# Performance work log

Measured on AMD Instinct MI355X. Metric: run time of the kernel, lower is better.

## Reference

```python
import math
import jax, jax.numpy as jnp
import numpy as np


def setup_inputs() -> dict:
    key = jax.random.key(0)
    T, C = 8192, 2048
    layer_depth, num_layers = 5, 10
    ks = jax.random.split(key, 8)

    x = jax.random.normal(ks[0], (T, C), jnp.float32)
    sx = jax.random.normal(ks[1], (C,), jnp.float32)
    aa = jnp.zeros((C,), jnp.float32)
    bb = jnp.zeros((C,), jnp.float32)
    pp = jnp.zeros((C,), jnp.float32)

    # parameter initial values per TimeMix.setup
    r01 = layer_depth / (num_layers - 1)
    r10 = 1.0 - layer_depth / num_layers
    zigzag = 0.5 * (jnp.arange(1, C + 1) % 3 - 1).astype(jnp.float32)
    time_first = jnp.full((C,), math.log(0.3), jnp.float32) + zigzag
    h = jnp.arange(C, dtype=jnp.float32)
    time_decay = (-5.0 + 8.0 * (h / (C - 1)) ** (0.7 + 1.3 * r01)).astype(jnp.float32)
    xr = jnp.arange(C, dtype=jnp.float32) / C
    time_mix_k = xr ** r10
    time_mix_v = time_mix_k + 0.3 * r01
    time_mix_r = xr ** (0.5 * r10)

    ln_scale = jnp.ones((C,), jnp.float32)
    ln_bias = jnp.zeros((C,), jnp.float32)

    s = 1.0 / np.sqrt(C)  # lecun-normal-ish scale for Dense kernels
    Wk = jax.random.normal(ks[2], (C, C), jnp.float32) * s
    Wv = jax.random.normal(ks[3], (C, C), jnp.float32) * s
    Wr = jax.random.normal(ks[4], (C, C), jnp.float32) * s
    Wo = jax.random.normal(ks[5], (C, C), jnp.float32) * s

    return dict(x=x, sx=sx, aa=aa, bb=bb, pp=pp,
                time_first=time_first, time_decay=time_decay,
                time_mix_k=time_mix_k, time_mix_v=time_mix_v, time_mix_r=time_mix_r,
                ln_scale=ln_scale, ln_bias=ln_bias,
                Wk=Wk, Wv=Wv, Wr=Wr, Wo=Wo)


def reference(x, sx, aa, bb, pp, time_first, time_decay,
              time_mix_k, time_mix_v, time_mix_r,
              ln_scale, ln_bias, Wk, Wv, Wr, Wo):
    # LayerNorm(eps=1e-5)
    mu = jnp.mean(x, axis=-1, keepdims=True)
    var = jnp.var(x, axis=-1, keepdims=True)
    xx = (x - mu) * jax.lax.rsqrt(var + 1e-5) * ln_scale + ln_bias  # [T, C]

    # token shift: previous timestep (sx state for t=0)
    sxs = jnp.concatenate((sx[None, :], xx[:-1, :]), axis=0)  # [T, C]
    kx = xx * time_mix_k + sxs * (1.0 - time_mix_k)
    vx = xx * time_mix_v + sxs * (1.0 - time_mix_v)
    rx = xx * time_mix_r + sxs * (1.0 - time_mix_r)

    r = jax.nn.sigmoid(rx @ Wr)  # [T, C]
    k = kx @ Wk                  # [T, C]
    v = vx @ Wv                  # [T, C]

    w = -jnp.exp(time_decay)     # [C]

    def step(state, kv):
        aa, bb, pp = state
        kk, vv = kv
        # output with numerically-stable log-sum-exp style bookkeeping
        ww = time_first + kk
        p = jnp.maximum(pp, ww)
        e1 = jnp.exp(pp - p)
        e2 = jnp.exp(ww - p)
        out = ((e1 * aa + e2 * vv) / (e1 * bb + e2)).astype(r.dtype)
        # state update
        ww2 = w + pp
        p2 = jnp.maximum(ww2, kk)
        e1b = jnp.exp(ww2 - p2)
        e2b = jnp.exp(kk - p2)
        aa = e1b * aa + e2b * vv
        bb = e1b * bb + e2b
        return (aa, bb, p2), out

    (aa, bb, pp), wkv = jax.lax.scan(step, (aa, bb, pp), (k, v))  # wkv: [T, C]

    out = x + (r * wkv) @ Wo
    return (out, xx[-1, :], aa, bb, pp)
```

## Files before the change

kernel.cpp:

```cpp
#include <hip/hip_runtime.h>
#include <stdint.h>

#define T_DIM 8192
#define C_DIM 2048
#define LCHUNK 128
#define NCHUNK (T_DIM / LCHUNK)

typedef unsigned short u16;
typedef __bf16 bf16x8_t __attribute__((ext_vector_type(8)));
typedef float f32x4_t __attribute__((ext_vector_type(4)));

__device__ __forceinline__ u16 f2bf(float f) {
    union { float f; uint32_t u; } x; x.f = f;
    uint32_t r = x.u + 0x7fffu + ((x.u >> 16) & 1u);
    return (u16)(r >> 16);
}
__device__ __forceinline__ float bf2f(u16 u) {
    union { uint32_t u; float f; } x; x.u = ((uint32_t)u) << 16;
    return x.f;
}
__device__ __forceinline__ void gload16(const void* g, void* l) {
    __builtin_amdgcn_global_load_lds((const __attribute__((address_space(1))) uint32_t*)g,
                                     (__attribute__((address_space(3))) uint32_t*)l, 16, 0, 0);
}
__device__ __forceinline__ f32x4_t mfma16(bf16x8_t a, bf16x8_t b, f32x4_t c) {
    return __builtin_amdgcn_mfma_f32_16x16x32_bf16(a, b, c, 0, 0, 0);
}

__device__ __forceinline__ void transpose_tile(const float* __restrict__ W, u16* __restrict__ Tm,
                                               int bn, int bk, float* shf)
{
    const int tid = threadIdx.x;
    const int tx = tid & 31, ty = tid >> 5;
#pragma unroll
    for (int i = 0; i < 4; ++i)
        shf[(ty + 8 * i) * 33 + tx] = W[(size_t)(bk + ty + 8 * i) * C_DIM + bn + tx];
    __syncthreads();
#pragma unroll
    for (int i = 0; i < 4; ++i)
        Tm[(size_t)(bn + ty + 8 * i) * C_DIM + bk + tx] = f2bf(shf[tx * 33 + ty + 8 * i]);
}

union F8 { float4 v[2]; float f[8]; };

__global__ __launch_bounds__(256)
void prep_kernel(const float* __restrict__ W0, const float* __restrict__ W1,
                 const float* __restrict__ W2, u16* __restrict__ Wt,
                 const float* __restrict__ x, const float* __restrict__ sx,
                 const float* __restrict__ lns, const float* __restrict__ lnb,
                 const float* __restrict__ tmk, const float* __restrict__ tmv,
                 const float* __restrict__ tmr,
                 u16* __restrict__ kx, u16* __restrict__ vx, u16* __restrict__ rx,
                 float* __restrict__ xx_last)
{
    __shared__ float shf[32 * 33];
    const int bid = blockIdx.x;
    const int tid = threadIdx.x;

    if (bid >= 8192) {
        const int z = (bid - 8192) >> 12;
        const int rem = (bid - 8192) & 4095;
        const float* W = (z == 0) ? W0 : (z == 1) ? W1 : W2;
        transpose_tile(W, Wt + (size_t)z * C_DIM * C_DIM, (rem & 63) * 32, (rem >> 6) * 32, shf);
        return;
    }

    const int t = bid;
    const size_t rowoff = (size_t)t * C_DIM;

    F8 a, p;
    const float4* xt = (const float4*)(x + rowoff);
    a.v[0] = xt[2 * tid]; a.v[1] = xt[2 * tid + 1];
    const float4* xp = (t == 0) ? (const float4*)sx : (const float4*)(x + rowoff - C_DIM);
    p.v[0] = xp[2 * tid]; p.v[1] = xp[2 * tid + 1];

    float s1 = 0.f, s2 = 0.f, s3 = 0.f, s4 = 0.f;
#pragma unroll
    for (int i = 0; i < 8; ++i) {
        s1 += a.f[i]; s2 += a.f[i] * a.f[i];
        s3 += p.f[i]; s4 += p.f[i] * p.f[i];
    }
#pragma unroll
    for (int off = 32; off; off >>= 1) {
        s1 += __shfl_down(s1, off);
        s2 += __shfl_down(s2, off);
        s3 += __shfl_down(s3, off);
        s4 += __shfl_down(s4, off);
    }
    float* red = shf;
    if ((tid & 63) == 0) {
        red[0 * 4 + (tid >> 6)] = s1; red[1 * 4 + (tid >> 6)] = s2;
        red[2 * 4 + (tid >> 6)] = s3; red[3 * 4 + (tid >> 6)] = s4;
    }
    __syncthreads();
    s1 = red[0] + red[1] + red[2] + red[3];
    s2 = red[4] + red[5] + red[6] + red[7];
    s3 = red[8] + red[9] + red[10] + red[11];
    s4 = red[12] + red[13] + red[14] + red[15];
    const float inv = 1.0f / (float)C_DIM;
    const float mu = s1 * inv;
    const float rstd = rsqrtf(s2 * inv - mu * mu + 1e-5f);
    const float mup = s3 * inv;
    const float rstdp = rsqrtf(s4 * inv - mup * mup + 1e-5f);

    F8 ls, lb, mk, mv, mr;
    { const float4* q = (const float4*)lns; ls.v[0] = q[2*tid]; ls.v[1] = q[2*tid+1]; }
    { const float4* q = (const float4*)lnb; lb.v[0] = q[2*tid]; lb.v[1] = q[2*tid+1]; }
    { const float4* q = (const float4*)tmk; mk.v[0] = q[2*tid]; mk.v[1] = q[2*tid+1]; }
    { const float4* q = (const float4*)tmv; mv.v[0] = q[2*tid]; mv.v[1] = q[2*tid+1]; }
    { const float4* q = (const float4*)tmr; mr.v[0] = q[2*tid]; mr.v[1] = q[2*tid+1]; }

    union { u16 u[8]; uint4 q; } ok, ov, orr;
#pragma unroll
    for (int i = 0; i < 8; ++i) {
        const float xxv  = (a.f[i] - mu) * rstd * ls.f[i] + lb.f[i];
        const float prev = (t == 0) ? p.f[i] : (p.f[i] - mup) * rstdp * ls.f[i] + lb.f[i];
        ok.u[i]  = f2bf(xxv * mk.f[i] + prev * (1.f - mk.f[i]));
        ov.u[i]  = f2bf(xxv * mv.f[i] + prev * (1.f - mv.f[i]));
        orr.u[i] = f2bf(xxv * mr.f[i] + prev * (1.f - mr.f[i]));
        if (t == T_DIM - 1) xx_last[tid * 8 + i] = xxv;
    }
    ((uint4*)(kx + rowoff))[tid] = ok.q;
    ((uint4*)(vx + rowoff))[tid] = ov.q;
    ((uint4*)(rx + rowoff))[tid] = orr.q;
}

__device__ __forceinline__ void gemm_core_sb(
    const u16* __restrict__ A, const u16* __restrict__ Bt,
    void* __restrict__ Cout, const int mode, const int N, const int K,
    const int m0, const int n0, u16* lds)
{
    const int tid = threadIdx.x;
    const int wave = tid >> 6, lane = tid & 63;
    const int wm = wave >> 1, wn = wave & 1;
    const int fr = lane & 15, fo = lane >> 4;
    const int sw = (fo ^ ((fr >> 1) & 3)) * 8;

    f32x4_t acc[4][4] = {};

    const int lrow = lane >> 2;
    const int scol = ((lane & 3) ^ ((lane >> 3) & 3)) * 8;
    const u16* gA = A  + (size_t)(m0 + wave * 16 + lrow) * K + scol;
    const u16* gB = Bt + (size_t)(n0 + wave * 16 + lrow) * K + scol;
    const size_t rk64 = (size_t)64 * K;
    const int dA = wave * 512;
    const int dB = 4096 + wave * 512;

    const int NT = K >> 5;
    for (int t = 0; t < NT; ++t) {
        const u16* ga = gA + (size_t)t * 32;
        const u16* gb = gB + (size_t)t * 32;
        gload16(ga,        lds + dA);
        gload16(ga + rk64, lds + dA + 2048);
        gload16(gb,        lds + dB);
        gload16(gb + rk64, lds + dB + 2048);
        __syncthreads();
        const u16* lA = lds + (wm * 64 + fr) * 32;
        const u16* lB = lds + 4096 + (wn * 64 + fr) * 32;
        bf16x8_t a[4], b[4];
#pragma unroll
        for (int i = 0; i < 4; ++i) {
            a[i] = *(const bf16x8_t*)(lA + i * 512 + sw);
            b[i] = *(const bf16x8_t*)(lB + i * 512 + sw);
        }
        __builtin_amdgcn_s_setprio(1);
#pragma unroll
        for (int mi = 0; mi < 4; ++mi)
#pragma unroll
            for (int ni = 0; ni < 4; ++ni)
                acc[mi][ni] = mfma16(a[mi], b[ni], acc[mi][ni]);
        __builtin_amdgcn_s_setprio(0);
        __syncthreads();
    }

    const int r4 = fo * 4;
#pragma unroll
    for (int mi = 0; mi < 4; ++mi) {
#pragma unroll
        for (int ni = 0; ni < 4; ++ni) {
            const int col = n0 + wn * 64 + ni * 16 + fr;
#pragma unroll
            for (int i = 0; i < 4; ++i) {
                const int row = m0 + wm * 64 + mi * 16 + r4 + i;
                float v = acc[mi][ni][i];
                if (mode == 1) ((u16*)Cout)[(size_t)row * N + col] = f2bf(v);
                else {
                    const float s = 1.f / (1.f + __expf(-v));
                    ((u16*)Cout)[(size_t)row * N + col] = f2bf(s);
                }
            }
        }
    }
}

__device__ __forceinline__ void gemm_core_db(
    const u16* __restrict__ A, const u16* __restrict__ Bt,
    float* __restrict__ Cout, const float* __restrict__ resid,
    const int N, const int K, const int m0, const int n0, u16* lds)
{
    const int tid = threadIdx.x;
    const int wave = tid >> 6, lane = tid & 63;
    const int wm = wave >> 1, wn = wave & 1;
    const int fr = lane & 15, fo = lane >> 4;
    const int sw = (fo ^ ((fr >> 1) & 3)) * 8;

    f32x4_t acc[4][4] = {};

    const int lrow = lane >> 2;
    const int scol = ((lane & 3) ^ ((lane >> 3) & 3)) * 8;
    const u16* gA = A  + (size_t)(m0 + wave * 16 + lrow) * K + scol;
    const u16* gB = Bt + (size_t)(n0 + wave * 16 + lrow) * K + scol;
    const size_t rk64 = (size_t)64 * K;
    const int dA = wave * 512;
    const int dB = 4096 + wave * 512;

    auto stage = [&](int t) {
        const int b = (t & 1) * 8192;
        const u16* ga = gA + (size_t)t * 32;
        const u16* gb = gB + (size_t)t * 32;
        gload16(ga,        lds + b + dA);
        gload16(ga + rk64, lds + b + dA + 2048);
        gload16(gb,        lds + b + dB);
        gload16(gb + rk64, lds + b + dB + 2048);
    };

    const int NT = K >> 5;
    stage(0);
    asm volatile("s_waitcnt vmcnt(0)" ::: "memory");
    asm volatile("s_barrier" ::: "memory");

    for (int t = 0; t < NT; ++t) {
        if (t + 1 < NT) stage(t + 1);
        const u16* lA = lds + (t & 1) * 8192 + (wm * 64 + fr) * 32;
        const u16* lB = lds + (t & 1) * 8192 + 4096 + (wn * 64 + fr) * 32;
        bf16x8_t a[4], b[4];
#pragma unroll
        for (int i = 0; i < 4; ++i) {
            a[i] = *(const bf16x8_t*)(lA + i * 512 + sw);
            b[i] = *(const bf16x8_t*)(lB + i * 512 + sw);
        }
        __builtin_amdgcn_s_setprio(1);
#pragma unroll
        for (int mi = 0; mi < 4; ++mi)
#pragma unroll
            for (int ni = 0; ni < 4; ++ni)
                acc[mi][ni] = mfma16(a[mi], b[ni], acc[mi][ni]);
        __builtin_amdgcn_s_setprio(0);
        asm volatile("s_waitcnt vmcnt(0)" ::: "memory");
        asm volatile("s_barrier" ::: "memory");
    }

    const int r4 = fo * 4;
#pragma unroll
    for (int mi = 0; mi < 4; ++mi) {
#pragma unroll
        for (int ni = 0; ni < 4; ++ni) {
            const int col = n0 + wn * 64 + ni * 16 + fr;
#pragma unroll
            for (int i = 0; i < 4; ++i) {
                const int row = m0 + wm * 64 + mi * 16 + r4 + i;
                Cout[(size_t)row * N + col] = acc[mi][ni][i] + resid[(size_t)row * N + col];
            }
        }
    }
}

__global__ __launch_bounds__(256, 4)
void gemm_kvr(const u16* __restrict__ kx, const u16* __restrict__ vx, const u16* __restrict__ rxp,
              const float* __restrict__ Wo, u16* __restrict__ Wt,
              u16* __restrict__ kbuf, u16* __restrict__ vbuf, u16* __restrict__ rbuf)
{
    __shared__ u16 lds[8192];
    const int bid = blockIdx.x;
    if (bid >= 3072) {
        const int rem = bid - 3072;
        transpose_tile(Wo, Wt + (size_t)3 * C_DIM * C_DIM, (rem & 63) * 32, (rem >> 6) * 32,
                       (float*)lds);
        return;
    }
    const int which = bid >> 10;
    const int b = bid & 1023;
    const int m0 = (b & 63) << 7;
    const int n0 = (b >> 6) << 7;
    const u16* A = (which == 0) ? kx : (which == 1) ? vx : rxp;
    const u16* B = Wt + (size_t)which * C_DIM * C_DIM;
    u16* C = (which == 0) ? kbuf : (which == 1) ? vbuf : rbuf;
    gemm_core_sb(A, B, C, (which == 2) ? 2 : 1, C_DIM, C_DIM, m0, n0, lds);
}

__global__ __launch_bounds__(256, 4)
void gemm_o(const u16* __restrict__ Aw, const u16* __restrict__ Wt3,
            float* __restrict__ out, const float* __restrict__ x)
{
    __shared__ u16 lds[16384];
    const int m0 = (int)(blockIdx.x & 63) << 7;
    const int n0 = (int)(blockIdx.x >> 6) << 7;
    gemm_core_db(Aw, Wt3, out, x, C_DIM, C_DIM, m0, n0, lds);
}

__global__ __launch_bounds__(256)
void scan_partial(const u16* __restrict__ k, const u16* __restrict__ v,
                  const float* __restrict__ time_decay,
                  float* __restrict__ pA, float* __restrict__ pB, float* __restrict__ pP)
{
    const int c = blockIdx.y * 256 + threadIdx.x;
    const int j = blockIdx.x;
    const float w = -__expf(time_decay[c]);
    float aa = 0.f, bb = 0.f, pp = -1e30f;
    const u16* kp = k + (size_t)j * LCHUNK * C_DIM + c;
    const u16* vp = v + (size_t)j * LCHUNK * C_DIM + c;
#pragma unroll 4
    for (int i = 0; i < LCHUNK; ++i) {
        const float kk = bf2f(*kp);
        const float vv = bf2f(*vp);
        kp += C_DIM; vp += C_DIM;
        const float ww = w + pp;
        const float p2 = fmaxf(ww, kk);
        const float e1 = __expf(ww - p2);
        const float e2 = __expf(kk - p2);
        aa = e1 * aa + e2 * vv;
        bb = e1 * bb + e2;
        pp = p2;
    }
    const int o = j * C_DIM + c;
    pA[o] = aa; pB[o] = bb; pP[o] = pp;
}

__global__ __launch_bounds__(256)
void scan_combine(const float* __restrict__ pA, const float* __restrict__ pB,
                  const float* __restrict__ pP,
                  const float* __restrict__ aa_in, const float* __restrict__ bb_in,
                  const float* __restrict__ pp_in,
                  const float* __restrict__ time_decay,
                  float* __restrict__ sA, float* __restrict__ sB, float* __restrict__ sP)
{
    const int c = blockIdx.x * 256 + threadIdx.x;
    const float wL = -__expf(time_decay[c]) * (float)LCHUNK;
    float a = aa_in[c], b = bb_in[c], p = pp_in[c];
    for (int j = 0; j < NCHUNK; ++j) {
        const int o = j * C_DIM + c;
        sA[o] = a; sB[o] = b; sP[o] = p;
        const float A = pA[o], B = pB[o], P = pP[o];
        const float pd = p + wL;
        const float q = fmaxf(pd, P);
        const float e1 = __expf(pd - q), e2 = __expf(P - q);
        a = e1 * a + e2 * A;
        b = e1 * b + e2 * B;
        p = q;
    }
}

__global__ __launch_bounds__(256)
void scan_out(const u16* __restrict__ k, const u16* __restrict__ v,
              const u16* __restrict__ r,
              const float* __restrict__ time_decay, const float* __restrict__ time_first,
              const float* __restrict__ sA, const float* __restrict__ sB,
              const float* __restrict__ sP,
              u16* __restrict__ arwkv,
              float* __restrict__ aa_out, float* __restrict__ bb_out, float* __restrict__ pp_out)
{
    const int c = blockIdx.y * 256 + threadIdx.x;
    const int j = blockIdx.x;
    const float w = -__expf(time_decay[c]);
    const float u = time_first[c];
    const int so = j * C_DIM + c;
    float aa = sA[so], bb = sB[so], pp = sP[so];
    const size_t base = (size_t)j * LCHUNK * C_DIM + c;
    const u16* kp = k + base;
    const u16* vp = v + base;
    const u16* rp = r + base;
    u16* op = arwkv + base;
#pragma unroll 4
    for (int i = 0; i < LCHUNK; ++i) {
        const float kk = bf2f(*kp);
        const float vv = bf2f(*vp);
        const float sr = bf2f(*rp);
        kp += C_DIM; vp += C_DIM; rp += C_DIM;
        const float ww = u + kk;
        const float p = fmaxf(pp, ww);
        const float e1 = __expf(pp - p);
        const float e2 = __expf(ww - p);
        const float out = (e1 * aa + e2 * vv) / (e1 * bb + e2);
        *op = f2bf(sr * out);
        op += C_DIM;
        const float ww2 = w + pp;
        const float p2 = fmaxf(ww2, kk);
        const float f1 = __expf(ww2 - p2);
        const float f2 = __expf(kk - p2);
        aa = f1 * aa + f2 * vv;
        bb = f1 * bb + f2;
        pp = p2;
    }
    if (j == NCHUNK - 1) { aa_out[c] = aa; bb_out[c] = bb; pp_out[c] = pp; }
}

extern "C" void kernel_launch(void* const* d_in, const int* in_sizes, int n_in,
                              void* d_out, int out_size, void* d_ws, size_t ws_size,
                              hipStream_t stream)
{
    (void)in_sizes; (void)n_in; (void)out_size; (void)ws_size;
    const float* x          = (const float*)d_in[0];
    const float* sx         = (const float*)d_in[1];
    const float* aa_in      = (const float*)d_in[2];
    const float* bb_in      = (const float*)d_in[3];
    const float* pp_in      = (const float*)d_in[4];
    const float* time_first = (const float*)d_in[5];
    const float* time_decay = (const float*)d_in[6];
    const float* tmk        = (const float*)d_in[7];
    const float* tmv        = (const float*)d_in[8];
    const float* tmr        = (const float*)d_in[9];
    const float* lns        = (const float*)d_in[10];
    const float* lnb        = (const float*)d_in[11];
    const float* Wk         = (const float*)d_in[12];
    const float* Wv         = (const float*)d_in[13];
    const float* Wr         = (const float*)d_in[14];
    const float* Wo         = (const float*)d_in[15];

    float* out     = (float*)d_out;
    float* xx_last = out + (size_t)T_DIM * C_DIM;
    float* aa_out  = xx_last + C_DIM;
    float* bb_out  = aa_out + C_DIM;
    float* pp_out  = bb_out + C_DIM;

    const size_t TC = (size_t)T_DIM * C_DIM;
    const size_t C2 = (size_t)C_DIM * C_DIM;
    u16* kx    = (u16*)d_ws;
    u16* vx    = kx + TC;
    u16* rx    = vx + TC;
    u16* Wt    = rx + TC;
    u16* kbuf  = Wt + 4 * C2;
    u16* vbuf  = kbuf + TC;
    u16* rbuf  = vbuf + TC;
    float* pA  = (float*)(rbuf + TC);
    float* pB  = pA + (size_t)NCHUNK * C_DIM;
    float* pP  = pB + (size_t)NCHUNK * C_DIM;
    float* sA  = pP + (size_t)NCHUNK * C_DIM;
    float* sB  = sA + (size_t)NCHUNK * C_DIM;
    float* sP  = sB + (size_t)NCHUNK * C_DIM;
    u16* arwkv = rx;

    prep_kernel<<<8192 + 12288, 256, 0, stream>>>(Wk, Wv, Wr, Wt,
                                                  x, sx, lns, lnb, tmk, tmv, tmr,
                                                  kx, vx, rx, xx_last);
    gemm_kvr<<<3072 + 4096, 256, 0, stream>>>(kx, vx, rx, Wo, Wt, kbuf, vbuf, rbuf);
    scan_partial<<<dim3(NCHUNK, C_DIM / 256), 256, 0, stream>>>(kbuf, vbuf, time_decay, pA, pB, pP);
    scan_combine<<<C_DIM / 256, 256, 0, stream>>>(pA, pB, pP, aa_in, bb_in, pp_in, time_decay, sA, sB, sP);
    scan_out<<<dim3(NCHUNK, C_DIM / 256), 256, 0, stream>>>(kbuf, vbuf, rbuf, time_decay, time_first,
                                                            sA, sB, sP, arwkv, aa_out, bb_out, pp_out);
    gemm_o<<<1024, 256, 0, stream>>>(arwkv, Wt + 3 * C2, out, x);
}
```

Baseline: 458.8 us.

## Vectorize chunked scan over 8 channels, shrink chunks, double-buffer KVR GEMM

The scan kernels now give each thread 8 adjacent channels, using 16-byte loads and stores instead of scalar 2-byte accesses. The chunk length drops from 128 to 32, which keeps the launch wide at NCHUNK blocks of 256 threads. The K/V/R projection GEMM now uses the double-buffered core already used for the output GEMM, at the cost of twice the LDS. The combine step prefetches the next chunk's partials, but it now runs a longer serial loop of 256 chunks per channel.

```diff
diff --git a/kernel.cpp b/kernel.cpp
--- a/kernel.cpp
+++ b/kernel.cpp
@@ -3,7 +3,7 @@
 
 #define T_DIM 8192
 #define C_DIM 2048
-#define LCHUNK 128
+#define LCHUNK 32
 #define NCHUNK (T_DIM / LCHUNK)
 
 typedef unsigned short u16;
@@ -125,78 +125,10 @@
     ((uint4*)(rx + rowoff))[tid] = orr.q;
 }
 
-__device__ __forceinline__ void gemm_core_sb(
-    const u16* __restrict__ A, const u16* __restrict__ Bt,
-    void* __restrict__ Cout, const int mode, const int N, const int K,
-    const int m0, const int n0, u16* lds)
-{
-    const int tid = threadIdx.x;
-    const int wave = tid >> 6, lane = tid & 63;
-    const int wm = wave >> 1, wn = wave & 1;
-    const int fr = lane & 15, fo = lane >> 4;
-    const int sw = (fo ^ ((fr >> 1) & 3)) * 8;
-
-    f32x4_t acc[4][4] = {};
-
-    const int lrow = lane >> 2;
-    const int scol = ((lane & 3) ^ ((lane >> 3) & 3)) * 8;
-    const u16* gA = A  + (size_t)(m0 + wave * 16 + lrow) * K + scol;
-    const u16* gB = Bt + (size_t)(n0 + wave * 16 + lrow) * K + scol;
-    const size_t rk64 = (size_t)64 * K;
-    const int dA = wave * 512;
-    const int dB = 4096 + wave * 512;
-
-    const int NT = K >> 5;
-    for (int t = 0; t < NT; ++t) {
-        const u16* ga = gA + (size_t)t * 32;
-        const u16* gb = gB + (size_t)t * 32;
-        gload16(ga,        lds + dA);
-        gload16(ga + rk64, lds + dA + 2048);
-        gload16(gb,        lds + dB);
-        gload16(gb + rk64, lds + dB + 2048);
-        __syncthreads();
-        const u16* lA = lds + (wm * 64 + fr) * 32;
-        const u16* lB = lds + 4096 + (wn * 64 + fr) * 32;
-        bf16x8_t a[4], b[4];
-#pragma unroll
-        for (int i = 0; i < 4; ++i) {
-            a[i] = *(const bf16x8_t*)(lA + i * 512 + sw);
-            b[i] = *(const bf16x8_t*)(lB + i * 512 + sw);
-        }
-        __builtin_amdgcn_s_setprio(1);
-#pragma unroll
-        for (int mi = 0; mi < 4; ++mi)
-#pragma unroll
-            for (int ni = 0; ni < 4; ++ni)
-                acc[mi][ni] = mfma16(a[mi], b[ni], acc[mi][ni]);
-        __builtin_amdgcn_s_setprio(0);
-        __syncthreads();
-    }
-
-    const int r4 = fo * 4;
-#pragma unroll
-    for (int mi = 0; mi < 4; ++mi) {
-#pragma unroll
-        for (int ni = 0; ni < 4; ++ni) {
-            const int col = n0 + wn * 64 + ni * 16 + fr;
-#pragma unroll
-            for (int i = 0; i < 4; ++i) {
-                const int row = m0 + wm * 64 + mi * 16 + r4 + i;
-                float v = acc[mi][ni][i];
-                if (mode == 1) ((u16*)Cout)[(size_t)row * N + col] = f2bf(v);
-                else {
-                    const float s = 1.f / (1.f + __expf(-v));
-                    ((u16*)Cout)[(size_t)row * N + col] = f2bf(s);
-                }
-            }
-        }
-    }
-}
-
 __device__ __forceinline__ void gemm_core_db(
     const u16* __restrict__ A, const u16* __restrict__ Bt,
-    float* __restrict__ Cout, const float* __restrict__ resid,
-    const int N, const int K, const int m0, const int n0, u16* lds)
+    void* __restrict__ Cout, const float* __restrict__ resid,
+    const int mode, const int N, const int K, const int m0, const int n0, u16* lds)
 {
     const int tid = threadIdx.x;
     const int wave = tid >> 6, lane = tid & 63;
@@ -259,7 +191,15 @@
 #pragma unroll
             for (int i = 0; i < 4; ++i) {
                 const int row = m0 + wm * 64 + mi * 16 + r4 + i;
-                Cout[(size_t)row * N + col] = acc[mi][ni][i] + resid[(size_t)row * N + col];
+                float v = acc[mi][ni][i];
+                if (mode == 0) {
+                    ((float*)Cout)[(size_t)row * N + col] = v + resid[(size_t)row * N + col];
+                } else if (mode == 1) {
+                    ((u16*)Cout)[(size_t)row * N + col] = f2bf(v);
+                } else {
+                    const float s = 1.f / (1.f + __expf(-v));
+                    ((u16*)Cout)[(size_t)row * N + col] = f2bf(s);
+                }
             }
         }
     }
@@ -270,7 +210,7 @@
               const float* __restrict__ Wo, u16* __restrict__ Wt,
               u16* __restrict__ kbuf, u16* __restrict__ vbuf, u16* __restrict__ rbuf)
 {
-    __shared__ u16 lds[8192];
+    __shared__ u16 lds[16384];
     const int bid = blockIdx.x;
     if (bid >= 3072) {
         const int rem = bid - 3072;
@@ -285,7 +225,7 @@
     const u16* A = (which == 0) ? kx : (which == 1) ? vx : rxp;
     const u16* B = Wt + (size_t)which * C_DIM * C_DIM;
     u16* C = (which == 0) ? kbuf : (which == 1) ? vbuf : rbuf;
-    gemm_core_sb(A, B, C, (which == 2) ? 2 : 1, C_DIM, C_DIM, m0, n0, lds);
+    gemm_core_db(A, B, C, nullptr, (which == 2) ? 2 : 1, C_DIM, C_DIM, m0, n0, lds);
 }
 
 __global__ __launch_bounds__(256, 4)
@@ -295,7 +235,7 @@
     __shared__ u16 lds[16384];
     const int m0 = (int)(blockIdx.x & 63) << 7;
     const int n0 = (int)(blockIdx.x >> 6) << 7;
-    gemm_core_db(Aw, Wt3, out, x, C_DIM, C_DIM, m0, n0, lds);
+    gemm_core_db(Aw, Wt3, out, x, 0, C_DIM, C_DIM, m0, n0, lds);
 }
 
 __global__ __launch_bounds__(256)
@@ -303,27 +243,45 @@
                   const float* __restrict__ time_decay,
                   float* __restrict__ pA, float* __restrict__ pB, float* __restrict__ pP)
 {
-    const int c = blockIdx.y * 256 + threadIdx.x;
     const int j = blockIdx.x;
-    const float w = -__expf(time_decay[c]);
-    float aa = 0.f, bb = 0.f, pp = -1e30f;
-    const u16* kp = k + (size_t)j * LCHUNK * C_DIM + c;
-    const u16* vp = v + (size_t)j * LCHUNK * C_DIM + c;
-#pragma unroll 4
-    for (int i = 0; i < LCHUNK; ++i) {
-        const float kk = bf2f(*kp);
-        const float vv = bf2f(*vp);
+    const int c0 = threadIdx.x * 8;
+    float w8[8];
+    {
+        F8 t; const float4* q = (const float4*)(time_decay + c0);
+        t.v[0] = q[0]; t.v[1] = q[1];
+#pragma unroll
+        for (int i = 0; i < 8; ++i) w8[i] = -__expf(t.f[i]);
+    }
+    float aa[8] = {}, bb[8] = {}, pp[8];
+#pragma unroll
+    for (int i = 0; i < 8; ++i) pp[i] = -1e30f;
+
+    const u16* kp = k + (size_t)j * LCHUNK * C_DIM + c0;
+    const u16* vp = v + (size_t)j * LCHUNK * C_DIM + c0;
+    for (int s = 0; s < LCHUNK; ++s) {
+        union { uint4 q; u16 u[8]; } kq, vq;
+        kq.q = *(const uint4*)kp; vq.q = *(const uint4*)vp;
         kp += C_DIM; vp += C_DIM;
-        const float ww = w + pp;
-        const float p2 = fmaxf(ww, kk);
-        const float e1 = __expf(ww - p2);
-        const float e2 = __expf(kk - p2);
-        aa = e1 * aa + e2 * vv;
-        bb = e1 * bb + e2;
-        pp = p2;
-    }
-    const int o = j * C_DIM + c;
-    pA[o] = aa; pB[o] = bb; pP[o] = pp;
+#pragma unroll
+        for (int i = 0; i < 8; ++i) {
+            const float kk = bf2f(kq.u[i]);
+            const float vv = bf2f(vq.u[i]);
+            const float ww = w8[i] + pp[i];
+            const float p2 = fmaxf(ww, kk);
+            const float e1 = __expf(ww - p2);
+            const float e2 = __expf(kk - p2);
+            aa[i] = e1 * aa[i] + e2 * vv;
+            bb[i] = e1 * bb[i] + e2;
+            pp[i] = p2;
+        }
+    }
+    const int o = j * C_DIM + c0;
+    *(float4*)(pA + o)     = make_float4(aa[0], aa[1], aa[2], aa[3]);
+    *(float4*)(pA + o + 4) = make_float4(aa[4], aa[5], aa[6], aa[7]);
+    *(float4*)(pB + o)     = make_float4(bb[0], bb[1], bb[2], bb[3]);
+    *(float4*)(pB + o + 4) = make_float4(bb[4], bb[5], bb[6], bb[7]);
+    *(float4*)(pP + o)     = make_float4(pp[0], pp[1], pp[2], pp[3]);
+    *(float4*)(pP + o + 4) = make_float4(pp[4], pp[5], pp[6], pp[7]);
 }
 
 __global__ __launch_bounds__(256)
@@ -337,16 +295,21 @@
     const int c = blockIdx.x * 256 + threadIdx.x;
     const float wL = -__expf(time_decay[c]) * (float)LCHUNK;
     float a = aa_in[c], b = bb_in[c], p = pp_in[c];
+    float A = pA[c], B = pB[c], P = pP[c];
     for (int j = 0; j < NCHUNK; ++j) {
         const int o = j * C_DIM + c;
+        float An = 0.f, Bn = 0.f, Pn = 0.f;
+        if (j + 1 < NCHUNK) {
+            An = pA[o + C_DIM]; Bn = pB[o + C_DIM]; Pn = pP[o + C_DIM];
+        }
         sA[o] = a; sB[o] = b; sP[o] = p;
-        const float A = pA[o], B = pB[o], P = pP[o];
         const float pd = p + wL;
         const float q = fmaxf(pd, P);
         const float e1 = __expf(pd - q), e2 = __expf(P - q);
         a = e1 * a + e2 * A;
         b = e1 * b + e2 * B;
         p = q;
+        A = An; B = Bn; P = Pn;
     }
 }
 
@@ -359,39 +322,71 @@
               u16* __restrict__ arwkv,
               float* __restrict__ aa_out, float* __restrict__ bb_out, float* __restrict__ pp_out)
 {
-    const int c = blockIdx.y * 256 + threadIdx.x;
     const int j = blockIdx.x;
-    const float w = -__expf(time_decay[c]);
-    const float u = time_first[c];
-    const int so = j * C_DIM + c;
-    float aa = sA[so], bb = sB[so], pp = sP[so];
-    const size_t base = (size_t)j * LCHUNK * C_DIM + c;
+    const int c0 = threadIdx.x * 8;
+    float w8[8], u8[8];
+    {
+        F8 t; const float4* q = (const float4*)(time_decay + c0);
+        t.v[0] = q[0]; t.v[1] = q[1];
+#pragma unroll
+        for (int i = 0; i < 8; ++i) w8[i] = -__expf(t.f[i]);
+        const float4* q2 = (const float4*)(time_first + c0);
+        t.v[0] = q2[0]; t.v[1] = q2[1];
+#pragma unroll
+        for (int i = 0; i < 8; ++i) u8[i] = t.f[i];
+    }
+    float aa[8], bb[8], pp[8];
+    {
+        const int so = j * C_DIM + c0;
+        F8 t;
+        t.v[0] = ((const float4*)(sA + so))[0]; t.v[1] = ((const float4*)(sA + so))[1];
+#pragma unroll
+        for (int i = 0; i < 8; ++i) aa[i] = t.f[i];
+        t.v[0] = ((const float4*)(sB + so))[0]; t.v[1] = ((const float4*)(sB + so))[1];
+#pragma unroll
+        for (int i = 0; i < 8; ++i) bb[i] = t.f[i];
+        t.v[0] = ((const float4*)(sP + so))[0]; t.v[1] = ((const float4*)(sP + so))[1];
+#pragma unroll
+        for (int i = 0; i < 8; ++i) pp[i] = t.f[i];
+    }
+
+    const size_t base = (size_t)j * LCHUNK * C_DIM + c0;
     const u16* kp = k + base;
     const u16* vp = v + base;
     const u16* rp = r + base;
     u16* op = arwkv + base;
-#pragma unroll 4
-    for (int i = 0; i < LCHUNK; ++i) {
-        const float kk = bf2f(*kp);
-        const float vv = bf2f(*vp);
-        const float sr = bf2f(*rp);
+    for (int s = 0; s < LCHUNK; ++s) {
+        union { uint4 q; u16 u[8]; } kq, vq, rq, oq;
+        kq.q = *(const uint4*)kp; vq.q = *(const uint4*)vp; rq.q = *(const uint4*)rp;
         kp += C_DIM; vp += C_DIM; rp += C_DIM;
-        const float ww = u + kk;
-        const float p = fmaxf(pp, ww);
-        const float e1 = __expf(pp - p);
-        const float e2 = __expf(ww - p);
-        const float out = (e1 * aa + e2 * vv) / (e1 * bb + e2);
-        *op = f2bf(sr * out);
+#pragma unroll
+        for (int i = 0; i < 8; ++i) {
+            const float kk = bf2f(kq.u[i]);
+            const float vv = bf2f(vq.u[i]);
+            const float sr = bf2f(rq.u[i]);
+            const float ww = u8[i] + kk;
+            const float p = fmaxf(pp[i], ww);
+            const float e1 = __expf(pp[i] - p);
+            const float e2 = __expf(ww - p);
+            const float o = (e1 * aa[i] + e2 * vv) / (e1 * bb[i] + e2);
+            oq.u[i] = f2bf(sr * o);
+            const float ww2 = w8[i] + pp[i];
+            const float p2 = fmaxf(ww2, kk);
+            const float f1 = __expf(ww2 - p2);
+            const float f2 = __expf(kk - p2);
+            aa[i] = f1 * aa[i] + f2 * vv;
+            bb[i] = f1 * bb[i] + f2;
+            pp[i] = p2;
+        }
+        *(uint4*)op = oq.q;
         op += C_DIM;
-        const float ww2 = w + pp;
-        const float p2 = fmaxf(ww2, kk);
-        const float f1 = __expf(ww2 - p2);
-        const float f2 = __expf(kk - p2);
-        aa = f1 * aa + f2 * vv;
-        bb = f1 * bb + f2;
-        pp = p2;
-    }
-    if (j == NCHUNK - 1) { aa_out[c] = aa; bb_out[c] = bb; pp_out[c] = pp; }
+    }
+    if (j == NCHUNK - 1) {
+#pragma unroll
+        for (int i = 0; i < 8; ++i) {
+            aa_out[c0 + i] = aa[i]; bb_out[c0 + i] = bb[i]; pp_out[c0 + i] = pp[i];
+        }
+    }
 }
 
 extern "C" void kernel_launch(void* const* d_in, const int* in_sizes, int n_in,
@@ -443,9 +438,9 @@
                                                   x, sx, lns, lnb, tmk, tmv, tmr,
                                                   kx, vx, rx, xx_last);
     gemm_kvr<<<3072 + 4096, 256, 0, stream>>>(kx, vx, rx, Wo, Wt, kbuf, vbuf, rbuf);
-    scan_partial<<<dim3(NCHUNK, C_DIM / 256), 256, 0, stream>>>(kbuf, vbuf, time_decay, pA, pB, pP);
+    scan_partial<<<NCHUNK, 256, 0, stream>>>(kbuf, vbuf, time_decay, pA, pB, pP);
     scan_combine<<<C_DIM / 256, 256, 0, stream>>>(pA, pB, pP, aa_in, bb_in, pp_in, time_decay, sA, sB, sP);
-    scan_out<<<dim3(NCHUNK, C_DIM / 256), 256, 0, stream>>>(kbuf, vbuf, rbuf, time_decay, time_first,
-                                                            sA, sB, sP, arwkv, aa_out, bb_out, pp_out);
+    scan_out<<<NCHUNK, 256, 0, stream>>>(kbuf, vbuf, rbuf, time_decay, time_first,
+                                         sA, sB, sP, arwkv, aa_out, bb_out, pp_out);
     gemm_o<<<1024, 256, 0, stream>>>(arwkv, Wt + 3 * C2, out, x);
 }
```

New measurement: 481.2 us. 4.9% more time.
